# Kernel tuning notes

Hardware: AMD Instinct MI355X
Metric: run time of the kernel (lower is better)

Reference implementation:

```python
import jax, jax.numpy as jnp
import numpy as np
import math

N_EMBD = 1024
N_HEAD = 16
HEAD_DIM = N_EMBD // N_HEAD


def setup_inputs() -> dict:
    key = jax.random.key(0)
    k_x, k_w1, k_b1, k_w2, k_b2 = jax.random.split(key, 5)
    B, T = 2, 2048
    x = jax.random.normal(k_x, (B, T, N_EMBD), dtype=jnp.float32)
    # ln1: Linear(n_embd, 3*n_embd); weights stored as [in, out] for x @ W
    W_qkv = jax.random.normal(k_w1, (N_EMBD, 3 * N_EMBD), dtype=jnp.float32) * 0.02
    b_qkv = jax.random.normal(k_b1, (3 * N_EMBD,), dtype=jnp.float32) * 0.02
    # ln2: Linear(n_embd, n_embd)
    W_out = jax.random.normal(k_w2, (N_EMBD, N_EMBD), dtype=jnp.float32) * 0.02
    b_out = jax.random.normal(k_b2, (N_EMBD,), dtype=jnp.float32) * 0.02
    return {"x": x, "W_qkv": W_qkv, "b_qkv": b_qkv, "W_out": W_out, "b_out": b_out}


def reference(x, W_qkv, b_qkv, W_out, b_out):
    B, T, C = x.shape
    qkv = x @ W_qkv + b_qkv                      # [B,T,3C]
    q, k, v = jnp.split(qkv, 3, axis=-1)
    # reshape to heads: [B, H, T, D]
    def to_heads(t):
        return t.reshape(B, T, N_HEAD, HEAD_DIM).transpose(0, 2, 1, 3)
    Q, K, V = to_heads(q), to_heads(k), to_heads(v)
    # NOTE: scale is 1/sqrt(n_head), as in the source (not sqrt(head_dim));
    # NOTE: no causal mask is applied, faithfully matching the source forward.
    scale = 1.0 / math.sqrt(N_HEAD)
    scores = jnp.einsum('bhqd,bhkd->bhqk', Q, K) * scale  # [B,H,T,T]
    attn = jax.nn.softmax(scores, axis=-1)
    out = jnp.einsum('bhqk,bhkd->bhqd', attn, V)          # [B,H,T,D]
    out = out.transpose(0, 2, 1, 3).reshape(B, T, C)
    # dropout = 0.0 -> identity (eval mode)
    return out @ W_out + b_out
```

## Files before the change

### kernel.cpp

```cpp
#include <hip/hip_runtime.h>
#include <hip/hip_bf16.h>
#include <stdint.h>

typedef __bf16 bf16_t;
typedef __bf16 bf16x8 __attribute__((ext_vector_type(8)));
typedef float  f32x4  __attribute__((ext_vector_type(4)));

#define AS1 __attribute__((address_space(1)))
#define AS3 __attribute__((address_space(3)))

__device__ __forceinline__ void gload16(const bf16_t* g, char* l) {
  __builtin_amdgcn_global_load_lds((AS1 const void*)(uintptr_t)g, (AS3 void*)l, 16, 0, 0);
}
__device__ __forceinline__ int swz8(int r) { return (r & 7) ^ ((r >> 2) & 6); }

#define C2S 0.36067376022224085f

__global__ void cvt_f32_bf16(const float* __restrict__ in, bf16_t* __restrict__ out, int n4) {
  int i = blockIdx.x * blockDim.x + threadIdx.x;
  if (i >= n4) return;
  float4 v = reinterpret_cast<const float4*>(in)[i];
  union { bf16_t h[4]; unsigned long long u; } r;
  r.h[0] = (bf16_t)v.x; r.h[1] = (bf16_t)v.y; r.h[2] = (bf16_t)v.z; r.h[3] = (bf16_t)v.w;
  reinterpret_cast<unsigned long long*>(out)[i] = r.u;
}

__global__ void trans_cvt(const float* __restrict__ W, bf16_t* __restrict__ Wt, int K, int N) {
  __shared__ float tile[32][33];
  const int kb = blockIdx.x * 32, nb = blockIdx.y * 32;
  const int tx = threadIdx.x, ty = threadIdx.y;
#pragma unroll
  for (int i = 0; i < 32; i += 8)
    tile[ty + i][tx] = W[(size_t)(kb + ty + i) * N + nb + tx];
  __syncthreads();
#pragma unroll
  for (int i = 0; i < 32; i += 8)
    Wt[(size_t)(nb + ty + i) * K + kb + tx] = (bf16_t)tile[tx][ty + i];
}

__global__ __launch_bounds__(256) void gemm_bt(
    const bf16_t* __restrict__ A, const bf16_t* __restrict__ Bt,
    const float* __restrict__ bias,
    bf16_t* __restrict__ outb, bf16_t* __restrict__ vtb, float* __restrict__ outf,
    int M, int N, int K, int ldo, int mode) {
  __shared__ bf16_t lA[128 * 32];
  __shared__ bf16_t lB[128 * 32];
  const int tid = threadIdx.x;
  const int wave = tid >> 6, lane = tid & 63;
  const int lr = lane & 15, lg = lane >> 4;
  const int ntiles = N >> 7;
  const int bn = blockIdx.x % ntiles, bm = blockIdx.x / ntiles;
  const int m0 = bm * 128, n0 = bn * 128;
  const int wr = wave >> 1, wc = wave & 1;
  f32x4 acc[4][4] = {};

  for (int k0 = 0; k0 < K; k0 += 32) {
    __syncthreads();
#pragma unroll
    for (int it = 0; it < 2; ++it) {
      const int wbase = it * 256 + wave * 64;
      const int lam = wbase + lane;
      const int row = lam >> 2;
      const int colb = ((lam & 3) << 4) ^ (((row >> 1) & 3) << 4);
      gload16(A  + (size_t)(m0 + row) * K + k0 + (colb >> 1), (char*)lA + wbase * 16);
      gload16(Bt + (size_t)(n0 + row) * K + k0 + (colb >> 1), (char*)lB + wbase * 16);
    }
    __syncthreads();

    bf16x8 af[4], bfv[4];
#pragma unroll
    for (int mi = 0; mi < 4; ++mi) {
      const int row = wr * 64 + mi * 16 + lr;
      af[mi] = *reinterpret_cast<const bf16x8*>(
          (const char*)lA + row * 64 + ((lg * 16) ^ (((row >> 1) & 3) << 4)));
    }
#pragma unroll
    for (int ni = 0; ni < 4; ++ni) {
      const int row = wc * 64 + ni * 16 + lr;
      bfv[ni] = *reinterpret_cast<const bf16x8*>(
          (const char*)lB + row * 64 + ((lg * 16) ^ (((row >> 1) & 3) << 4)));
    }
    __builtin_amdgcn_s_setprio(1);
#pragma unroll
    for (int mi = 0; mi < 4; ++mi)
#pragma unroll
      for (int ni = 0; ni < 4; ++ni)
        acc[mi][ni] = __builtin_amdgcn_mfma_f32_16x16x32_bf16(af[mi], bfv[ni], acc[mi][ni], 0, 0, 0);
    __builtin_amdgcn_s_setprio(0);
  }

#pragma unroll
  for (int mi = 0; mi < 4; ++mi) {
#pragma unroll
    for (int ni = 0; ni < 4; ++ni) {
      const int col = n0 + wc * 64 + ni * 16 + lr;
      const float bv = bias[col];
      const int rg0 = m0 + wr * 64 + mi * 16 + lg * 4;
      if (mode == 1 && col >= 2048) {
        const int colv = col - 2048;
        const int dd = colv & 63, hh = colv >> 6;
        const int bb = rg0 >> 11, t = rg0 & 2047;
        union { bf16_t h4[4]; unsigned long long u; } pk;
#pragma unroll
        for (int r = 0; r < 4; ++r) pk.h4[r] = (bf16_t)(acc[mi][ni][r] + bv);
        *reinterpret_cast<unsigned long long*>(
            vtb + (size_t)(bb * 16 + hh) * 131072 + (size_t)dd * 2048 + t) = pk.u;
      } else {
        const float sc = (mode == 1 && col < 1024) ? C2S : 1.f;
#pragma unroll
        for (int r = 0; r < 4; ++r) {
          const float v = (acc[mi][ni][r] + bv) * sc;
          if (mode == 2) outf[(size_t)(rg0 + r) * ldo + col] = v;
          else           outb[(size_t)(rg0 + r) * ldo + col] = (bf16_t)v;
        }
      }
    }
  }
}

__global__ __launch_bounds__(256) void attn_fwd(
    const bf16_t* __restrict__ qkv2,
    const bf16_t* __restrict__ vT,
    bf16_t* __restrict__ a0, bf16_t* __restrict__ a1,
    float* __restrict__ lbuf) {
  __shared__ bf16_t lds[2][8192];
  const int tid = threadIdx.x;
  const int wave = tid >> 6, lane = tid & 63;
  const int lr = lane & 15, lg = lane >> 4;
  const int id = blockIdx.x;
  const int xcd = id & 7, slot = id >> 3;
  const int bh = xcd * 4 + (slot & 3);
  const int rest = slot >> 2;
  const int qb = rest & 15, kvh = rest >> 4;
  const int b = bh >> 4, h = bh & 15;

  const int q0 = qb * 128 + wave * 32;
  const bf16_t* Qp = qkv2 + (size_t)(b * 2048 + q0) * 2048 + h * 64;
  bf16x8 qf[2][2];
#pragma unroll
  for (int hx = 0; hx < 2; ++hx) {
    qf[hx][0] = *reinterpret_cast<const bf16x8*>(Qp + (size_t)(hx * 16 + lr) * 2048 + lg * 8);
    qf[hx][1] = *reinterpret_cast<const bf16x8*>(Qp + (size_t)(hx * 16 + lr) * 2048 + 32 + lg * 8);
  }

  const int kr0 = tid >> 3;
  const int ks  = (tid & 7) ^ swz8(kr0);
  const bf16_t* Ks0 = qkv2 + (size_t)(b * 2048 + kvh * 1024 + kr0) * 2048 + 1024 + h * 64 + ks * 8;
  const bf16_t* Ks1 = Ks0 + (size_t)32 * 2048;
  const bf16_t* Vs0 = vT + (size_t)bh * 131072 + (size_t)kr0 * 2048 + kvh * 1024 + ks * 8;
  const bf16_t* Vs1 = Vs0 + (size_t)32 * 2048;

  auto stage = [&](int buf, int kb) {
    char* base = (char*)&lds[buf][0] + wave * 1024;
    gload16(Ks0 + (size_t)kb * 131072, base);
    gload16(Ks1 + (size_t)kb * 131072, base + 4096);
    gload16(Vs0 + (size_t)kb * 64, base + 8192);
    gload16(Vs1 + (size_t)kb * 64, base + 12288);
  };

  int kofs[4][2], vofs[4][2];
#pragma unroll
  for (int t = 0; t < 4; ++t) {
    const int kk = 32 * (t >> 1) + 8 * (lr >> 2) + 4 * (t & 1) + (lr & 3);
    const int sw = swz8(kk) << 4;
    kofs[t][0] = (kk << 7) + ((lg * 16) ^ sw);
    kofs[t][1] = (kk << 7) + ((64 + lg * 16) ^ sw);
  }
#pragma unroll
  for (int nc = 0; nc < 4; ++nc) {
    const int vr = nc * 16 + lr;
    const int sw = swz8(vr) << 4;
    vofs[nc][0] = 8192 + (vr << 7) + ((lg * 16) ^ sw);
    vofs[nc][1] = 8192 + (vr << 7) + ((64 + lg * 16) ^ sw);
  }

  f32x4 acc[2][4] = {};
  f32x4 lac[2] = {};

  int cur = 0;
  stage(0, 0);
  __syncthreads();

  for (int kb = 0; kb < 16; ++kb) {
    if (kb < 15) stage(cur ^ 1, kb + 1);
    const char* bK = (const char*)&lds[cur][0];

    f32x4 s[2][4];
#pragma unroll
    for (int t = 0; t < 4; ++t) {
      const bf16x8 k0 = *reinterpret_cast<const bf16x8*>(bK + kofs[t][0]);
      const bf16x8 k1 = *reinterpret_cast<const bf16x8*>(bK + kofs[t][1]);
#pragma unroll
      for (int hx = 0; hx < 2; ++hx) {
        f32x4 z = {0.f, 0.f, 0.f, 0.f};
        z = __builtin_amdgcn_mfma_f32_16x16x32_bf16(k0, qf[hx][0], z, 0, 0, 0);
        s[hx][t] = __builtin_amdgcn_mfma_f32_16x16x32_bf16(k1, qf[hx][1], z, 0, 0, 0);
      }
    }

    bf16x8 pa[2][2];
#pragma unroll
    for (int hx = 0; hx < 2; ++hx) {
      float p[16];
#pragma unroll
      for (int t = 0; t < 4; ++t)
#pragma unroll
        for (int r = 0; r < 4; ++r) {
          p[t * 4 + r] = __builtin_amdgcn_exp2f(s[hx][t][r]);
          lac[hx][r] += p[t * 4 + r];
        }
#pragma unroll
      for (int j = 0; j < 8; ++j) { pa[hx][0][j] = (bf16_t)p[j]; pa[hx][1][j] = (bf16_t)p[8 + j]; }
    }

#pragma unroll
    for (int nc = 0; nc < 4; ++nc) {
      const bf16x8 v0 = *reinterpret_cast<const bf16x8*>(bK + vofs[nc][0]);
      const bf16x8 v1 = *reinterpret_cast<const bf16x8*>(bK + vofs[nc][1]);
#pragma unroll
      for (int hx = 0; hx < 2; ++hx) {
        acc[hx][nc] = __builtin_amdgcn_mfma_f32_16x16x32_bf16(pa[hx][0], v0, acc[hx][nc], 0, 0, 0);
        acc[hx][nc] = __builtin_amdgcn_mfma_f32_16x16x32_bf16(pa[hx][1], v1, acc[hx][nc], 0, 0, 0);
      }
    }

    __syncthreads();
    cur ^= 1;
  }

  bf16_t* ap = kvh ? a1 : a0;
#pragma unroll
  for (int hx = 0; hx < 2; ++hx) {
    float lsum = (lac[hx][0] + lac[hx][1]) + (lac[hx][2] + lac[hx][3]);
    lsum += __shfl_xor(lsum, 16);
    lsum += __shfl_xor(lsum, 32);
    const float li = 1.f / lsum;
#pragma unroll
    for (int r = 0; r < 4; ++r) {
      const float lf = __shfl(li, lg * 4 + r);
      const int qg = q0 + hx * 16 + lg * 4 + r;
      bf16_t* op = ap + (size_t)(b * 2048 + qg) * 1024 + h * 64 + lr;
#pragma unroll
      for (int nc = 0; nc < 4; ++nc) op[nc * 16] = (bf16_t)(acc[hx][nc][r] * lf);
    }
    if (lane < 16)
      lbuf[(size_t)(kvh * 4096 + b * 2048 + q0 + hx * 16 + lane) * 16 + h] = lsum;
  }
}

__global__ void attn_reduce(const bf16_t* __restrict__ a0, const bf16_t* __restrict__ a1,
                            const float* __restrict__ lbuf, bf16_t* __restrict__ aout) {
  const int i = blockIdx.x * 256 + threadIdx.x;
  const int r = i >> 7, h = (i & 127) >> 3;
  const float l0 = lbuf[(size_t)r * 16 + h];
  const float l1 = lbuf[(size_t)(4096 + r) * 16 + h];
  const float inv = 1.f / (l0 + l1);
  const float w0 = l0 * inv, w1 = l1 * inv;
  const bf16x8 v0 = reinterpret_cast<const bf16x8*>(a0)[i];
  const bf16x8 v1 = reinterpret_cast<const bf16x8*>(a1)[i];
  bf16x8 o;
#pragma unroll
  for (int j = 0; j < 8; ++j) o[j] = (bf16_t)(w0 * (float)v0[j] + w1 * (float)v1[j]);
  reinterpret_cast<bf16x8*>(aout)[i] = o;
}

extern "C" void kernel_launch(void* const* d_in, const int* in_sizes, int n_in,
                              void* d_out, int out_size, void* d_ws, size_t ws_size,
                              hipStream_t stream) {
  (void)in_sizes; (void)n_in; (void)out_size; (void)ws_size;
  const float* x    = (const float*)d_in[0];
  const float* Wqkv = (const float*)d_in[1];
  const float* bqkv = (const float*)d_in[2];
  const float* Wout = (const float*)d_in[3];
  const float* bout = (const float*)d_in[4];
  float* out = (float*)d_out;

  char* ws = (char*)d_ws;
  bf16_t* xb    = (bf16_t*)(ws);
  bf16_t* a0    = (bf16_t*)(ws);
  bf16_t* wqkvT = (bf16_t*)(ws + 8388608);
  bf16_t* woutT = (bf16_t*)(ws + 14680064);
  bf16_t* qkv2  = (bf16_t*)(ws + 16777216);
  bf16_t* aout  = (bf16_t*)(ws + 16777216);
  bf16_t* vT    = (bf16_t*)(ws + 33554432);
  bf16_t* a1    = (bf16_t*)(ws + 41943040);
  float*  lbuf  = (float*)(ws + 50331648);

  cvt_f32_bf16<<<4096, 256, 0, stream>>>(x, xb, 1048576);
  trans_cvt<<<dim3(32, 96), dim3(32, 8), 0, stream>>>(Wqkv, wqkvT, 1024, 3072);
  trans_cvt<<<dim3(32, 32), dim3(32, 8), 0, stream>>>(Wout, woutT, 1024, 1024);
  gemm_bt<<<768, 256, 0, stream>>>(xb, wqkvT, bqkv, qkv2, vT, nullptr, 4096, 3072, 1024, 2048, 1);
  attn_fwd<<<1024, 256, 0, stream>>>(qkv2, vT, a0, a1, lbuf);
  attn_reduce<<<2048, 256, 0, stream>>>(a0, a1, lbuf, aout);
  gemm_bt<<<256, 256, 0, stream>>>(aout, woutT, bout, nullptr, nullptr, out, 4096, 1024, 1024, 1024, 2);
}
```

Before: 133.0 us.

## Use 512-thread attention blocks, MFMA row sums, wave priority, XCD-aware GEMM order

The attention kernel now runs 8 waves per block over 256 query rows, so each K/V tile staged in LDS serves twice as many queries and each thread issues half as many loads. The softmax row sums are computed with extra MFMAs against a vector of ones instead of VALU adds plus cross-lane shuffles. s_setprio is raised around the MFMA section. GEMM block IDs are remapped so consecutive tiles land on the same XCD, for better L2 locality. The costs are more MFMA work, half as many attention blocks in flight, and larger blocks that may reduce occupancy.

```diff
diff --git a/kernel.cpp b/kernel.cpp
--- a/kernel.cpp
+++ b/kernel.cpp
@@ -49,7 +49,8 @@
   const int wave = tid >> 6, lane = tid & 63;
   const int lr = lane & 15, lg = lane >> 4;
   const int ntiles = N >> 7;
-  const int bn = blockIdx.x % ntiles, bm = blockIdx.x / ntiles;
+  const int bid = (blockIdx.x & 7) * ((int)gridDim.x >> 3) + (blockIdx.x >> 3);
+  const int bn = bid % ntiles, bm = bid / ntiles;
   const int m0 = bm * 128, n0 = bn * 128;
   const int wr = wave >> 1, wc = wave & 1;
   f32x4 acc[4][4] = {};
@@ -118,7 +119,7 @@
   }
 }
 
-__global__ __launch_bounds__(256) void attn_fwd(
+__global__ __launch_bounds__(512) void attn_fwd(
     const bf16_t* __restrict__ qkv2,
     const bf16_t* __restrict__ vT,
     bf16_t* __restrict__ a0, bf16_t* __restrict__ a1,
@@ -131,10 +132,10 @@
   const int xcd = id & 7, slot = id >> 3;
   const int bh = xcd * 4 + (slot & 3);
   const int rest = slot >> 2;
-  const int qb = rest & 15, kvh = rest >> 4;
+  const int qb = rest & 7, kvh = rest >> 3;
   const int b = bh >> 4, h = bh & 15;
 
-  const int q0 = qb * 128 + wave * 32;
+  const int q0 = qb * 256 + wave * 32;
   const bf16_t* Qp = qkv2 + (size_t)(b * 2048 + q0) * 2048 + h * 64;
   bf16x8 qf[2][2];
 #pragma unroll
@@ -143,19 +144,15 @@
     qf[hx][1] = *reinterpret_cast<const bf16x8*>(Qp + (size_t)(hx * 16 + lr) * 2048 + 32 + lg * 8);
   }
 
-  const int kr0 = tid >> 3;
-  const int ks  = (tid & 7) ^ swz8(kr0);
-  const bf16_t* Ks0 = qkv2 + (size_t)(b * 2048 + kvh * 1024 + kr0) * 2048 + 1024 + h * 64 + ks * 8;
-  const bf16_t* Ks1 = Ks0 + (size_t)32 * 2048;
-  const bf16_t* Vs0 = vT + (size_t)bh * 131072 + (size_t)kr0 * 2048 + kvh * 1024 + ks * 8;
-  const bf16_t* Vs1 = Vs0 + (size_t)32 * 2048;
+  const int kr = tid >> 3;
+  const int ks = (tid & 7) ^ swz8(kr);
+  const bf16_t* Ksrc = qkv2 + (size_t)(b * 2048 + kvh * 1024 + kr) * 2048 + 1024 + h * 64 + ks * 8;
+  const bf16_t* Vsrc = vT + (size_t)bh * 131072 + (size_t)kr * 2048 + kvh * 1024 + ks * 8;
 
   auto stage = [&](int buf, int kb) {
     char* base = (char*)&lds[buf][0] + wave * 1024;
-    gload16(Ks0 + (size_t)kb * 131072, base);
-    gload16(Ks1 + (size_t)kb * 131072, base + 4096);
-    gload16(Vs0 + (size_t)kb * 64, base + 8192);
-    gload16(Vs1 + (size_t)kb * 64, base + 12288);
+    gload16(Ksrc + (size_t)kb * 131072, base);
+    gload16(Vsrc + (size_t)kb * 64, base + 8192);
   };
 
   int kofs[4][2], vofs[4][2];
@@ -175,7 +172,10 @@
   }
 
   f32x4 acc[2][4] = {};
-  f32x4 lac[2] = {};
+  f32x4 accl[2] = {};
+  bf16x8 ones;
+#pragma unroll
+  for (int j = 0; j < 8; ++j) ones[j] = (bf16_t)1.0f;
 
   int cur = 0;
   stage(0, 0);
@@ -205,12 +205,17 @@
 #pragma unroll
       for (int t = 0; t < 4; ++t)
 #pragma unroll
-        for (int r = 0; r < 4; ++r) {
+        for (int r = 0; r < 4; ++r)
           p[t * 4 + r] = __builtin_amdgcn_exp2f(s[hx][t][r]);
-          lac[hx][r] += p[t * 4 + r];
-        }
 #pragma unroll
       for (int j = 0; j < 8; ++j) { pa[hx][0][j] = (bf16_t)p[j]; pa[hx][1][j] = (bf16_t)p[8 + j]; }
+    }
+
+    __builtin_amdgcn_s_setprio(1);
+#pragma unroll
+    for (int hx = 0; hx < 2; ++hx) {
+      accl[hx] = __builtin_amdgcn_mfma_f32_16x16x32_bf16(pa[hx][0], ones, accl[hx], 0, 0, 0);
+      accl[hx] = __builtin_amdgcn_mfma_f32_16x16x32_bf16(pa[hx][1], ones, accl[hx], 0, 0, 0);
     }
 
 #pragma unroll
@@ -223,6 +228,7 @@
         acc[hx][nc] = __builtin_amdgcn_mfma_f32_16x16x32_bf16(pa[hx][1], v1, acc[hx][nc], 0, 0, 0);
       }
     }
+    __builtin_amdgcn_s_setprio(0);
 
     __syncthreads();
     cur ^= 1;
@@ -231,20 +237,16 @@
   bf16_t* ap = kvh ? a1 : a0;
 #pragma unroll
   for (int hx = 0; hx < 2; ++hx) {
-    float lsum = (lac[hx][0] + lac[hx][1]) + (lac[hx][2] + lac[hx][3]);
-    lsum += __shfl_xor(lsum, 16);
-    lsum += __shfl_xor(lsum, 32);
-    const float li = 1.f / lsum;
 #pragma unroll
     for (int r = 0; r < 4; ++r) {
-      const float lf = __shfl(li, lg * 4 + r);
+      const float lf = 1.f / accl[hx][r];
       const int qg = q0 + hx * 16 + lg * 4 + r;
       bf16_t* op = ap + (size_t)(b * 2048 + qg) * 1024 + h * 64 + lr;
 #pragma unroll
       for (int nc = 0; nc < 4; ++nc) op[nc * 16] = (bf16_t)(acc[hx][nc][r] * lf);
-    }
-    if (lane < 16)
-      lbuf[(size_t)(kvh * 4096 + b * 2048 + q0 + hx * 16 + lane) * 16 + h] = lsum;
+      if (lr == 0)
+        lbuf[(size_t)(kvh * 4096 + b * 2048 + qg) * 16 + h] = accl[hx][r];
+    }
   }
 }
 
@@ -290,7 +292,7 @@
   trans_cvt<<<dim3(32, 96), dim3(32, 8), 0, stream>>>(Wqkv, wqkvT, 1024, 3072);
   trans_cvt<<<dim3(32, 32), dim3(32, 8), 0, stream>>>(Wout, woutT, 1024, 1024);
   gemm_bt<<<768, 256, 0, stream>>>(xb, wqkvT, bqkv, qkv2, vT, nullptr, 4096, 3072, 1024, 2048, 1);
-  attn_fwd<<<1024, 256, 0, stream>>>(qkv2, vT, a0, a1, lbuf);
+  attn_fwd<<<512, 512, 0, stream>>>(qkv2, vT, a0, a1, lbuf);
   attn_reduce<<<2048, 256, 0, stream>>>(a0, a1, lbuf, aout);
   gemm_bt<<<256, 256, 0, stream>>>(aout, woutT, bout, nullptr, nullptr, out, 4096, 1024, 1024, 1024, 2);
 }
```

Result: faster. 122.9 us (-7.6%).
